# Performance work log

Hardware: AMD Instinct MI355X
Metric: run time of the kernel (lower is better)

The kernel has to match this reference:

```python
import jax, jax.numpy as jnp
import numpy as np


def setup_inputs() -> dict:
    key = jax.random.key(0)
    k1, k2, k3 = jax.random.split(key, 3)
    B, T, D, U = 256, 1024, 128, 256
    x = jax.random.normal(k1, (B, T, D), dtype=jnp.float32)
    h0 = jnp.zeros((B, U), dtype=jnp.float32)
    W = jax.random.normal(k2, (D + U, U), dtype=jnp.float32) * 0.05
    bias = jax.random.normal(k3, (U,), dtype=jnp.float32) * 0.05
    return {"x": x, "h0": h0, "W": W, "bias": bias}


def reference(x, h0, W, bias):
    # x: [B, T, D], h0: [B, U], W: [D+U, U], bias: [U]
    # Per step: Ht = tanh(concat([Ht, x_t], -1) @ W + bias)
    U = h0.shape[-1]
    Wh = W[:U]   # [U, U] part multiplying the state (concat order is (Ht, inputs))
    Wx = W[U:]   # [D, U] part multiplying the input
    # Precompute input projections for all timesteps in one big GEMM.
    x_proj = jnp.einsum('btd,du->btu', x, Wx) + bias  # [B, T, U]

    def step(h, xp_t):
        h_new = jnp.tanh(h @ Wh + xp_t)
        return h_new, h_new

    # scan over time: xs must be time-major
    _, hs = jax.lax.scan(step, h0, jnp.swapaxes(x_proj, 0, 1))  # hs: [T, B, U]
    return jnp.swapaxes(hs, 0, 1)  # [B, T, U]
```

## Files before the change

### kernel.cpp

```cpp
#include <hip/hip_runtime.h>


typedef _Float16 half8 __attribute__((ext_vector_type(8)));
typedef _Float16 half4v __attribute__((ext_vector_type(4)));
typedef float floatx4 __attribute__((ext_vector_type(4)));

constexpr int B = 256, T = 1024, D = 128, U = 256;
constexpr int NSL = (U + D) / 32;
constexpr int QS  = 16 * 16 + 16;
constexpr int SS  = 4 * QS;
constexpr int BUF = NSL * SS;

constexpr float TANH_K = 2.8853900817779268f;

__device__ __forceinline__ float fexp2(float v) {
#if __has_builtin(__builtin_amdgcn_exp2f)
    return __builtin_amdgcn_exp2f(v);
#else
    return exp2f(v);
#endif
}
__device__ __forceinline__ float frcp(float v) {
#if __has_builtin(__builtin_amdgcn_rcpf)
    return __builtin_amdgcn_rcpf(v);
#else
    return 1.0f / v;
#endif
}
__device__ __forceinline__ float tanh_prescaled(float a) {
    float e = fexp2(a);
    return 1.0f - 2.0f * frcp(e + 1.0f);
}

__device__ __forceinline__ void cvt_write8(void* dst, float4 lo, float4 hi) {
    half8 h;
    h[0] = (_Float16)lo.x; h[1] = (_Float16)lo.y;
    h[2] = (_Float16)lo.z; h[3] = (_Float16)lo.w;
    h[4] = (_Float16)hi.x; h[5] = (_Float16)hi.y;
    h[6] = (_Float16)hi.z; h[7] = (_Float16)hi.w;
    *reinterpret_cast<half8*>(dst) = h;
}
__device__ __forceinline__ void cvt_write4(void* dst, float4 v) {
    half4v h;
    h[0] = (_Float16)v.x; h[1] = (_Float16)v.y;
    h[2] = (_Float16)v.z; h[3] = (_Float16)v.w;
    *reinterpret_cast<half4v*>(dst) = h;
}

__global__ __launch_bounds__(512, 2)
void rnn_mfma_kernel(const float* __restrict__ x, const float* __restrict__ h0,
                     const float* __restrict__ W, const float* __restrict__ bias,
                     float* __restrict__ out)
{
    __shared__ __align__(16) unsigned char lds[2 * BUF];

    const int tid  = threadIdx.x;
    const int lane = tid & 63;
    const int wv   = tid >> 6;
    const int l15  = lane & 15;
    const int quad = lane >> 4;
    const int b0   = blockIdx.x * 16;

    half8 wf[2][NSL];
    float bv[2];
#pragma unroll
    for (int nt = 0; nt < 2; ++nt) {
        const int n = 32 * wv + 16 * nt + l15;
        bv[nt] = bias[n] * TANH_K;
#pragma unroll
        for (int s = 0; s < NSL; ++s) {
            half8 f;
#pragma unroll
            for (int j = 0; j < 8; ++j) {
                const int k = 32 * s + 8 * quad + j;
                f[j] = (_Float16)(W[(size_t)k * U + n] * TANH_K);
            }
            wf[nt][s] = f;
        }
    }

    {
        const int hm = tid >> 5;
        const int cc = tid & 31;
        const float* hp = h0 + (size_t)(b0 + hm) * U + 8 * cc;
        cvt_write8(lds + (cc >> 2) * SS + (cc & 3) * QS + hm * 16,
                   *reinterpret_cast<const float4*>(hp),
                   *reinterpret_cast<const float4*>(hp + 4));
    }
    const int sm = tid >> 5;
    const int f4 = tid & 31;
    const int c8 = f4 >> 1;
    const float* xbase = x + (size_t)(b0 + sm) * T * D + 4 * f4;
    const int xslot = (8 + (c8 >> 2)) * SS + (c8 & 3) * QS + sm * 16 + (f4 & 1) * 8;
    cvt_write4(lds + xslot, *reinterpret_cast<const float4*>(xbase));

    float4 p = *reinterpret_cast<const float4*>(xbase + D);
    float4 q;

    __syncthreads();

    const int aoff = quad * QS + l15 * 16;

    floatx4 acc0[2];
#pragma unroll
    for (int nt = 0; nt < 2; ++nt)
        acc0[nt] = (floatx4){bv[nt], bv[nt], bv[nt], bv[nt]};
    float* optr[8];
    int    pubo[8];
#pragma unroll
    for (int i = 0; i < 8; ++i) {
        const int nt = i >> 2, r = i & 3;
        const int n = 32 * wv + 16 * nt + l15;
        const int m = 4 * quad + r;
        optr[i] = out + (size_t)(b0 + m) * T * U + n;
        pubo[i] = (n >> 5) * SS + ((n >> 3) & 3) * QS + m * 16 + (n & 7) * 2;
    }

#define STEP(tt, CO, NO, PP, QQ)                                               \
    do {                                                                       \
        const int t_ = (tt);                                                   \
        const int tp_ = (t_ + 2 < T) ? (t_ + 2) : (T - 1);                     \
        QQ = *reinterpret_cast<const float4*>(xbase + (size_t)D * tp_);        \
        const unsigned char* ab = lds + (CO) + aoff;                           \
        half8 ax[4];                                                           \
        _Pragma("unroll")                                                      \
        for (int s = 0; s < 4; ++s)                                            \
            ax[s] = *reinterpret_cast<const half8*>(ab + (8 + s) * SS);        \
        half8 ah[8];                                                           \
        _Pragma("unroll")                                                      \
        for (int s = 0; s < 8; ++s)                                            \
            ah[s] = *reinterpret_cast<const half8*>(ab + s * SS);              \
        floatx4 acc[2];                                                        \
        acc[0] = acc0[0]; acc[1] = acc0[1];                                    \
        __builtin_amdgcn_s_setprio(1);                                         \
        _Pragma("unroll")                                                      \
        for (int s = 0; s < 4; ++s)                                            \
            _Pragma("unroll")                                                  \
            for (int nt = 0; nt < 2; ++nt)                                     \
                acc[nt] = __builtin_amdgcn_mfma_f32_16x16x32_f16(              \
                              ax[s], wf[nt][8 + s], acc[nt], 0, 0, 0);         \
        _Pragma("unroll")                                                      \
        for (int s = 0; s < 8; ++s)                                            \
            _Pragma("unroll")                                                  \
            for (int nt = 0; nt < 2; ++nt)                                     \
                acc[nt] = __builtin_amdgcn_mfma_f32_16x16x32_f16(              \
                              ah[s], wf[nt][s], acc[nt], 0, 0, 0);             \
        __builtin_amdgcn_s_setprio(0);                                         \
        float hv[8];                                                           \
        _Pragma("unroll")                                                      \
        for (int i = 0; i < 8; ++i)                                            \
            hv[i] = tanh_prescaled(acc[i >> 2][i & 3]);                        \
                                     \
        _Pragma("unroll")                                                      \
        for (int i = 0; i < 8; ++i)                                            \
            optr[i][(size_t)t_ * U] = hv[i];                                   \
                \
        _Pragma("unroll")                                                      \
        for (int i = 0; i < 8; ++i)                                            \
            *reinterpret_cast<_Float16*>(lds + (NO) + pubo[i]) =               \
                (_Float16)hv[i];                                               \
        cvt_write4(lds + (NO) + xslot, PP);                                    \
        __syncthreads();                                                       \
    } while (0)

    for (int t = 0; t < T; t += 2) {
        STEP(t,     0,   BUF, p, q);
        STEP(t + 1, BUF, 0,   q, p);
    }
#undef STEP
}

extern "C" void kernel_launch(void* const* d_in, const int* in_sizes, int n_in,
                              void* d_out, int out_size, void* d_ws, size_t ws_size,
                              hipStream_t stream) {
    const float* x    = (const float*)d_in[0];
    const float* h0   = (const float*)d_in[1];
    const float* W    = (const float*)d_in[2];
    const float* bias = (const float*)d_in[3];
    float* out = (float*)d_out;

    hipLaunchKernelGGL(rnn_mfma_kernel, dim3(B / 16), dim3(512), 0, stream,
                       x, h0, W, bias, out);
}
```

Baseline: 1.083 ms.

## Precompute input projection in separate MFMA kernel, stage it through output buffer

Moves the x@Wx+bias projection out of the serial recurrence into a separate fully parallel MFMA kernel that writes prescaled projections into the output buffer. The recurrent kernel then reads each step's projection from out (prefetched two steps ahead) as the accumulator initialiser and only does the 256-wide Wh MFMAs. This shortens the serial per-step critical path (fewer MFMAs, no x staging in LDS) at the cost of an extra full pass writing and reading B*T*U floats through global memory.

Result: slower. 1.337 ms (+23.5%).

```diff
diff --git a/kernel.cpp b/kernel.cpp
--- a/kernel.cpp
+++ b/kernel.cpp
@@ -2,11 +2,10 @@
 
 
 typedef _Float16 half8 __attribute__((ext_vector_type(8)));
-typedef _Float16 half4v __attribute__((ext_vector_type(4)));
 typedef float floatx4 __attribute__((ext_vector_type(4)));
 
 constexpr int B = 256, T = 1024, D = 128, U = 256;
-constexpr int NSL = (U + D) / 32;
+constexpr int NSL = U / 32;
 constexpr int QS  = 16 * 16 + 16;
 constexpr int SS  = 4 * QS;
 constexpr int BUF = NSL * SS;
@@ -40,16 +39,76 @@
     h[6] = (_Float16)hi.z; h[7] = (_Float16)hi.w;
     *reinterpret_cast<half8*>(dst) = h;
 }
-__device__ __forceinline__ void cvt_write4(void* dst, float4 v) {
-    half4v h;
-    h[0] = (_Float16)v.x; h[1] = (_Float16)v.y;
-    h[2] = (_Float16)v.z; h[3] = (_Float16)v.w;
-    *reinterpret_cast<half4v*>(dst) = h;
+
+__global__ __launch_bounds__(256, 2)
+void xproj_kernel(const float* __restrict__ x, const float* __restrict__ W,
+                  const float* __restrict__ bias, float* __restrict__ out)
+{
+    const int tid  = threadIdx.x;
+    const int lane = tid & 63;
+    const int wv   = tid >> 6;
+    const int l15  = lane & 15;
+    const int quad = lane >> 4;
+    const size_t r0 = (size_t)blockIdx.x * 64;
+
+    half8 wf[4][4];
+    float bv[4];
+#pragma unroll
+    for (int nt = 0; nt < 4; ++nt) {
+        const int n = 64 * wv + 16 * nt + l15;
+        bv[nt] = bias[n] * TANH_K;
+#pragma unroll
+        for (int s = 0; s < 4; ++s) {
+            half8 f;
+#pragma unroll
+            for (int j = 0; j < 8; ++j) {
+                const int d = 32 * s + 8 * quad + j;
+                f[j] = (_Float16)(W[(size_t)(U + d) * U + n] * TANH_K);
+            }
+            wf[nt][s] = f;
+        }
+    }
+
+#pragma unroll
+    for (int rt = 0; rt < 4; ++rt) {
+        const size_t row = r0 + 16 * rt + l15;
+        const float* xr = x + row * D + 8 * quad;
+        half8 a[4];
+#pragma unroll
+        for (int s = 0; s < 4; ++s) {
+            float4 lo = *reinterpret_cast<const float4*>(xr + 32 * s);
+            float4 hi = *reinterpret_cast<const float4*>(xr + 32 * s + 4);
+            half8 f;
+            f[0] = (_Float16)lo.x; f[1] = (_Float16)lo.y;
+            f[2] = (_Float16)lo.z; f[3] = (_Float16)lo.w;
+            f[4] = (_Float16)hi.x; f[5] = (_Float16)hi.y;
+            f[6] = (_Float16)hi.z; f[7] = (_Float16)hi.w;
+            a[s] = f;
+        }
+        floatx4 acc[4];
+#pragma unroll
+        for (int nt = 0; nt < 4; ++nt)
+            acc[nt] = (floatx4){bv[nt], bv[nt], bv[nt], bv[nt]};
+#pragma unroll
+        for (int s = 0; s < 4; ++s)
+#pragma unroll
+            for (int nt = 0; nt < 4; ++nt)
+                acc[nt] = __builtin_amdgcn_mfma_f32_16x16x32_f16(
+                              a[s], wf[nt][s], acc[nt], 0, 0, 0);
+#pragma unroll
+        for (int nt = 0; nt < 4; ++nt) {
+            const int n = 64 * wv + 16 * nt + l15;
+#pragma unroll
+            for (int r = 0; r < 4; ++r) {
+                const size_t orow = r0 + 16 * rt + 4 * quad + r;
+                out[orow * U + n] = acc[nt][r];
+            }
+        }
+    }
 }
 
 __global__ __launch_bounds__(512, 2)
-void rnn_mfma_kernel(const float* __restrict__ x, const float* __restrict__ h0,
-                     const float* __restrict__ W, const float* __restrict__ bias,
+void rnn_mfma_kernel(const float* __restrict__ h0, const float* __restrict__ W,
                      float* __restrict__ out)
 {
     __shared__ __align__(16) unsigned char lds[2 * BUF];
@@ -62,11 +121,9 @@
     const int b0   = blockIdx.x * 16;
 
     half8 wf[2][NSL];
-    float bv[2];
 #pragma unroll
     for (int nt = 0; nt < 2; ++nt) {
         const int n = 32 * wv + 16 * nt + l15;
-        bv[nt] = bias[n] * TANH_K;
 #pragma unroll
         for (int s = 0; s < NSL; ++s) {
             half8 f;
@@ -87,24 +144,7 @@
                    *reinterpret_cast<const float4*>(hp),
                    *reinterpret_cast<const float4*>(hp + 4));
     }
-    const int sm = tid >> 5;
-    const int f4 = tid & 31;
-    const int c8 = f4 >> 1;
-    const float* xbase = x + (size_t)(b0 + sm) * T * D + 4 * f4;
-    const int xslot = (8 + (c8 >> 2)) * SS + (c8 & 3) * QS + sm * 16 + (f4 & 1) * 8;
-    cvt_write4(lds + xslot, *reinterpret_cast<const float4*>(xbase));
-
-    float4 p = *reinterpret_cast<const float4*>(xbase + D);
-    float4 q;
-
-    __syncthreads();
-
-    const int aoff = quad * QS + l15 * 16;
-
-    floatx4 acc0[2];
-#pragma unroll
-    for (int nt = 0; nt < 2; ++nt)
-        acc0[nt] = (floatx4){bv[nt], bv[nt], bv[nt], bv[nt]};
+
     float* optr[8];
     int    pubo[8];
 #pragma unroll
@@ -116,31 +156,34 @@
         pubo[i] = (n >> 5) * SS + ((n >> 3) & 3) * QS + m * 16 + (n & 7) * 2;
     }
 
-#define STEP(tt, CO, NO, PP, QQ)                                               \
+    float xa[8], xb[8];
+#pragma unroll
+    for (int i = 0; i < 8; ++i) xa[i] = optr[i][0];
+#pragma unroll
+    for (int i = 0; i < 8; ++i) xb[i] = optr[i][U];
+
+    __syncthreads();
+
+    const int aoff = quad * QS + l15 * 16;
+
+#define STEP(tt, CO, NO, XR)                                                   \
     do {                                                                       \
         const int t_ = (tt);                                                   \
+        floatx4 acc[2];                                                        \
+        acc[0] = (floatx4){XR[0], XR[1], XR[2], XR[3]};                        \
+        acc[1] = (floatx4){XR[4], XR[5], XR[6], XR[7]};                        \
         const int tp_ = (t_ + 2 < T) ? (t_ + 2) : (T - 1);                     \
-        QQ = *reinterpret_cast<const float4*>(xbase + (size_t)D * tp_);        \
+        _Pragma("unroll")                                                      \
+        for (int i = 0; i < 8; ++i)                                            \
+            XR[i] = optr[i][(size_t)tp_ * U];                                  \
         const unsigned char* ab = lds + (CO) + aoff;                           \
-        half8 ax[4];                                                           \
-        _Pragma("unroll")                                                      \
-        for (int s = 0; s < 4; ++s)                                            \
-            ax[s] = *reinterpret_cast<const half8*>(ab + (8 + s) * SS);        \
-        half8 ah[8];                                                           \
-        _Pragma("unroll")                                                      \
-        for (int s = 0; s < 8; ++s)                                            \
+        half8 ah[NSL];                                                         \
+        _Pragma("unroll")                                                      \
+        for (int s = 0; s < NSL; ++s)                                          \
             ah[s] = *reinterpret_cast<const half8*>(ab + s * SS);              \
-        floatx4 acc[2];                                                        \
-        acc[0] = acc0[0]; acc[1] = acc0[1];                                    \
         __builtin_amdgcn_s_setprio(1);                                         \
         _Pragma("unroll")                                                      \
-        for (int s = 0; s < 4; ++s)                                            \
-            _Pragma("unroll")                                                  \
-            for (int nt = 0; nt < 2; ++nt)                                     \
-                acc[nt] = __builtin_amdgcn_mfma_f32_16x16x32_f16(              \
-                              ax[s], wf[nt][8 + s], acc[nt], 0, 0, 0);         \
-        _Pragma("unroll")                                                      \
-        for (int s = 0; s < 8; ++s)                                            \
+        for (int s = 0; s < NSL; ++s)                                          \
             _Pragma("unroll")                                                  \
             for (int nt = 0; nt < 2; ++nt)                                     \
                 acc[nt] = __builtin_amdgcn_mfma_f32_16x16x32_f16(              \
@@ -154,18 +197,17 @@
         _Pragma("unroll")                                                      \
         for (int i = 0; i < 8; ++i)                                            \
             optr[i][(size_t)t_ * U] = hv[i];                                   \
-                \
+                           \
         _Pragma("unroll")                                                      \
         for (int i = 0; i < 8; ++i)                                            \
             *reinterpret_cast<_Float16*>(lds + (NO) + pubo[i]) =               \
                 (_Float16)hv[i];                                               \
-        cvt_write4(lds + (NO) + xslot, PP);                                    \
         __syncthreads();                                                       \
     } while (0)
 
     for (int t = 0; t < T; t += 2) {
-        STEP(t,     0,   BUF, p, q);
-        STEP(t + 1, BUF, 0,   q, p);
+        STEP(t,     0,   BUF, xa);
+        STEP(t + 1, BUF, 0,   xb);
     }
 #undef STEP
 }
@@ -179,6 +221,8 @@
     const float* bias = (const float*)d_in[3];
     float* out = (float*)d_out;
 
+    hipLaunchKernelGGL(xproj_kernel, dim3((B * T) / 64), dim3(256), 0, stream,
+                       x, W, bias, out);
     hipLaunchKernelGGL(rnn_mfma_kernel, dim3(B / 16), dim3(512), 0, stream,
-                       x, h0, W, bias, out);
-}
+                       h0, W, out);
+}
```
